# Kernel tuning notes

Hardware: AMD Instinct MI355X
Metric: run time of the kernel (lower is better)

The kernel has to match this reference:

```python
import jax, jax.numpy as jnp
import numpy as np

NEG_SLOPE = 0.2  # LeakyReLU slope used by standard GAT


def setup_inputs() -> dict:
    key = jax.random.key(0)
    k1, k2, k3, k4, k5, k6 = jax.random.split(key, 6)
    N, E, F_in, F_out = 100000, 1600000, 256, 128
    x = jax.random.normal(k1, (N, F_in), dtype=jnp.float32)
    edge_index = jax.random.randint(k2, (2, E), 0, N, dtype=jnp.int32)
    W = jax.random.normal(k3, (F_in, F_out), dtype=jnp.float32) * (1.0 / np.sqrt(F_in))
    a_src = jax.random.normal(k4, (F_out,), dtype=jnp.float32) * 0.1
    a_dst = jax.random.normal(k5, (F_out,), dtype=jnp.float32) * 0.1
    return {"x": x, "edge_index": edge_index, "W": W, "a_src": a_src, "a_dst": a_dst}


def reference(x, edge_index, W, a_src, a_dst):
    N = x.shape[0]
    src, dst = edge_index[0], edge_index[1]

    Wh = x @ W                               # [N, F_out]
    alpha_src = Wh @ a_src                   # [N]
    alpha_dst = Wh @ a_dst                   # [N]

    e = alpha_src[src] + alpha_dst[dst]      # [E] raw edge scores
    e = jnp.where(e > 0, e, NEG_SLOPE * e)   # LeakyReLU(0.2)

    # segment softmax over incoming edges of each destination node
    seg_max = jax.ops.segment_max(e, dst, num_segments=N)          # [N]
    seg_max = jnp.where(jnp.isfinite(seg_max), seg_max, 0.0)
    e_exp = jnp.exp(e - seg_max[dst])                               # [E]
    denom = jax.ops.segment_sum(e_exp, dst, num_segments=N)         # [N]
    alpha = e_exp / (denom[dst] + 1e-16)                            # [E]

    # weighted aggregation of source messages
    msgs = alpha[:, None] * Wh[src]                                  # [E, F_out]
    out = jax.ops.segment_sum(msgs, dst, num_segments=N)             # [N, F_out]
    return jax.nn.elu(out)
```

## Files before the change

### kernel.cpp

```cpp
#include <hip/hip_runtime.h>
#include <math.h>

#define NEG_SLOPE 0.2f
#define BINSH 8
#define BCAP 6144

typedef __attribute__((ext_vector_type(8))) short bf16x8;
typedef __attribute__((ext_vector_type(4))) float f32x4;
typedef __attribute__((ext_vector_type(8))) unsigned short us8;

__device__ inline unsigned short f2b(float f) {
  union { float f; unsigned u; } v; v.f = f;
  unsigned r = v.u + 0x7fffu + ((v.u >> 16) & 1u);
  return (unsigned short)(r >> 16);
}

__device__ inline void gload_lds16(const float* g, void* l) {
  __builtin_amdgcn_global_load_lds(
      (const __attribute__((address_space(1))) void*)g,
      (__attribute__((address_space(3))) void*)l, 16, 0, 0);
}

__launch_bounds__(256)
__global__ void k_work1(const float* __restrict__ W, unsigned short* __restrict__ WtBs,
                        const int* __restrict__ src, const int* __restrict__ dst,
                        int* __restrict__ cursor, unsigned* __restrict__ binned,
                        int E, int NBUK) {
  int bid = blockIdx.x;
  int t = threadIdx.x;
  if (bid < 128) {
    int i = bid * 256 + t;
    int k = i >> 7, n = i & 127;
    int c = k >> 3, e = k & 7;
    WtBs[n * 256 + ((c ^ (n & 31)) << 3) + e] = f2b(W[(size_t)k * 128 + n]);
    return;
  }
  __shared__ int lh[512];
  for (int c = t; c < NBUK; c += 256) lh[c] = 0;
  __syncthreads();
  int base = (bid - 128) * 2048;
  int bq[8], rq[8]; unsigned pq[8];
#pragma unroll
  for (int q = 0; q < 8; ++q) {
    int j = base + q * 256 + t;
    if (j < E) {
      int d = dst[j], s = src[j];
      bq[q] = d >> BINSH;
      pq[q] = ((unsigned)s << 8) | (unsigned)(d & 255);
      rq[q] = atomicAdd(&lh[bq[q]], 1);
    } else bq[q] = -1;
  }
  __syncthreads();
  for (int c = t; c < NBUK; c += 256) { int cnt = lh[c]; if (cnt) lh[c] = atomicAdd(&cursor[c], cnt); }
  __syncthreads();
#pragma unroll
  for (int q = 0; q < 8; ++q)
    if (bq[q] >= 0) binned[(size_t)bq[q] * BCAP + lh[bq[q]] + rq[q]] = pq[q];
}

__launch_bounds__(512, 4)
__global__ void k_work2(const float* __restrict__ x, const unsigned short* __restrict__ WtBs,
                        const float* __restrict__ a_src, const float* __restrict__ a_dst,
                        unsigned short* __restrict__ WhB, float* __restrict__ asrc,
                        float* __restrict__ adst, int N, int nGemm,
                        const unsigned* __restrict__ binned, const int* __restrict__ cursor,
                        int* __restrict__ offsets, int* __restrict__ degs,
                        int* __restrict__ csr) {
  __shared__ __align__(16) unsigned char sbuf[65536];
  int t = threadIdx.x;
  if ((int)blockIdx.x < nGemm) {
    unsigned short* Bs = (unsigned short*)sbuf;
    unsigned short* Cs = (unsigned short*)sbuf;
    int lane = t & 63, wid = t >> 6;
    int lr = lane & 15, lh2 = lane >> 4;
    int m0 = blockIdx.x * 256;

#pragma unroll
    for (int i = 0; i < 8; ++i) {
      int chunk = i * 512 + t;
      gload_lds16((const float*)WtBs + (size_t)chunk * 4, (char*)sbuf + (size_t)chunk * 16);
    }

    int row0 = m0 + wid * 32 + lr;
    int row1 = row0 + 16;
    int r0c = row0 < N ? row0 : N - 1;
    int r1c = row1 < N ? row1 : N - 1;
    const float* xp0 = x + (size_t)r0c * 256 + lh2 * 8;
    const float* xp1 = x + (size_t)r1c * 256 + lh2 * 8;

    f32x4 acc[2][8];
#pragma unroll
    for (int rf = 0; rf < 2; ++rf)
#pragma unroll
      for (int f = 0; f < 8; ++f) acc[rf][f] = (f32x4){0.f, 0.f, 0.f, 0.f};

    __syncthreads();

#pragma unroll
    for (int ks = 0; ks < 8; ++ks) {
      float4 u0 = *(const float4*)(xp0 + ks * 32);
      float4 u1 = *(const float4*)(xp0 + ks * 32 + 4);
      float4 v0 = *(const float4*)(xp1 + ks * 32);
      float4 v1 = *(const float4*)(xp1 + ks * 32 + 4);
      bf16x8 a0, a1;
      a0[0] = (short)f2b(u0.x); a0[1] = (short)f2b(u0.y);
      a0[2] = (short)f2b(u0.z); a0[3] = (short)f2b(u0.w);
      a0[4] = (short)f2b(u1.x); a0[5] = (short)f2b(u1.y);
      a0[6] = (short)f2b(u1.z); a0[7] = (short)f2b(u1.w);
      a1[0] = (short)f2b(v0.x); a1[1] = (short)f2b(v0.y);
      a1[2] = (short)f2b(v0.z); a1[3] = (short)f2b(v0.w);
      a1[4] = (short)f2b(v1.x); a1[5] = (short)f2b(v1.y);
      a1[6] = (short)f2b(v1.z); a1[7] = (short)f2b(v1.w);
#pragma unroll
      for (int f = 0; f < 8; ++f) {
        int n = lr + 16 * f;
        bf16x8 b = *(const bf16x8*)(Bs + n * 256 + (((ks * 4 + lh2) ^ (n & 31)) << 3));
        acc[0][f] = __builtin_amdgcn_mfma_f32_16x16x32_bf16(a0, b, acc[0][f], 0, 0, 0);
        acc[1][f] = __builtin_amdgcn_mfma_f32_16x16x32_bf16(a1, b, acc[1][f], 0, 0, 0);
      }
    }

    float asv[8], adv[8];
#pragma unroll
    for (int f = 0; f < 8; ++f) { asv[f] = a_src[lr + 16 * f]; adv[f] = a_dst[lr + 16 * f]; }
    float as_p[2][4] = {}, ad_p[2][4] = {};
#pragma unroll
    for (int rf = 0; rf < 2; ++rf)
#pragma unroll
      for (int f = 0; f < 8; ++f)
#pragma unroll
        for (int r = 0; r < 4; ++r) {
          as_p[rf][r] += acc[rf][f][r] * asv[f];
          ad_p[rf][r] += acc[rf][f][r] * adv[f];
        }
#pragma unroll
    for (int off = 1; off < 16; off <<= 1)
#pragma unroll
      for (int rf = 0; rf < 2; ++rf)
#pragma unroll
        for (int r = 0; r < 4; ++r) {
          as_p[rf][r] += __shfl_xor(as_p[rf][r], off);
          ad_p[rf][r] += __shfl_xor(ad_p[rf][r], off);
        }
    if (lr == 0) {
#pragma unroll
      for (int rf = 0; rf < 2; ++rf)
#pragma unroll
        for (int r = 0; r < 4; ++r) {
          int m = m0 + wid * 32 + rf * 16 + lh2 * 4 + r;
          if (m < N) { asrc[m] = as_p[rf][r]; adst[m] = ad_p[rf][r]; }
        }
    }

#pragma unroll
    for (int h = 0; h < 2; ++h) {
      __syncthreads();
      if ((wid >> 2) == h) {
#pragma unroll
        for (int rf = 0; rf < 2; ++rf)
#pragma unroll
          for (int f = 0; f < 8; ++f)
#pragma unroll
            for (int r = 0; r < 4; ++r)
              Cs[((wid & 3) * 32 + rf * 16 + lh2 * 4 + r) * 136 + lr + 16 * f] =
                  f2b(acc[rf][f][r]);
      }
      __syncthreads();
#pragma unroll
      for (int i = 0; i < 4; ++i) {
        int chunk = i * 512 + t;
        int row = chunk >> 4, c8 = chunk & 15;
        int m = m0 + h * 128 + row;
        if (m < N)
          *(us8*)(WhB + (size_t)m * 128 + c8 * 8) = *(const us8*)(Cs + row * 136 + c8 * 8);
      }
    }
    return;
  }

  {
    int b = blockIdx.x - nGemm;
    int beg = b * BCAP, end = beg + cursor[b];
    int node0 = b << BINSH;
    int nn = N - node0; if (nn > 256) nn = 256; if (nn < 0) nn = 0;
    int* ldeg = (int*)sbuf;
    int* lcur = ldeg + 256;
    int* wp = lcur + 256;
    if (t < 256) ldeg[t] = 0;
    __syncthreads();
    for (int j = beg + t; j < end; j += 512) atomicAdd(&ldeg[binned[j] & 255u], 1);
    __syncthreads();
    if (t < 256) {
      int lane = t & 63, wid = t >> 6;
      int v = (t < nn) ? ldeg[t] : 0;
      int incl = v;
#pragma unroll
      for (int off = 1; off < 64; off <<= 1) { int u = __shfl_up(incl, off); if (lane >= off) incl += u; }
      if (lane == 63) wp[wid] = incl;
      lcur[t] = incl - v;
    }
    __syncthreads();
    if (t < 256) {
      int wid = t >> 6;
      int add = 0;
      for (int k = 0; k < wid; ++k) add += wp[k];
      int ex = add + lcur[t];
      int v = (t < nn) ? ldeg[t] : 0;
      if (t < nn) { offsets[node0 + t] = beg + ex; degs[node0 + t] = v; }
      lcur[t] = ex;
    }
    __syncthreads();
    for (int j = beg + t; j < end; j += 512) {
      unsigned e = binned[j];
      int r = atomicAdd(&lcur[e & 255u], 1);
      csr[beg + r] = (int)(e >> 8);
    }
  }
}

__launch_bounds__(256)
__global__ void k_agg(const int* __restrict__ csr, const int* __restrict__ offsets,
                      const int* __restrict__ degs,
                      const unsigned short* __restrict__ WhB, const float* __restrict__ asrc,
                      const float* __restrict__ adst, float* __restrict__ out, int N) {
  int gt = blockIdx.x * blockDim.x + threadIdx.x;
  int wave = gt >> 6;
  int lane = gt & 63;
  int lq = lane & 15;
  int g = lane >> 4;
  int node = wave * 4 + g;
  if (node >= N) return;
  int beg = offsets[node];
  int end = beg + degs[node];
  float ad = adst[node];
  float acc[8] = {};
  float psum = 0.f;
  for (int chunk = beg; chunk < end; chunk += 16) {
    int j = chunk + lq;
    float p = 0.f; int mys = 0;
    if (j < end) {
      mys = csr[j];
      float e = asrc[mys] + ad;
      e = e > 0.f ? e : NEG_SLOPE * e;
      p = __expf(e);
    }
    psum += p;
#pragma unroll
    for (int tt = 0; tt < 8; ++tt) {
      float pt = __shfl(p, tt, 16);
      int st = __shfl(mys, tt, 16);
      uint4 v = *(const uint4*)(WhB + (size_t)(unsigned)st * 128u + lq * 8);
      acc[0] = fmaf(pt, __uint_as_float(v.x << 16), acc[0]);
      acc[1] = fmaf(pt, __uint_as_float(v.x & 0xffff0000u), acc[1]);
      acc[2] = fmaf(pt, __uint_as_float(v.y << 16), acc[2]);
      acc[3] = fmaf(pt, __uint_as_float(v.y & 0xffff0000u), acc[3]);
      acc[4] = fmaf(pt, __uint_as_float(v.z << 16), acc[4]);
      acc[5] = fmaf(pt, __uint_as_float(v.z & 0xffff0000u), acc[5]);
      acc[6] = fmaf(pt, __uint_as_float(v.w << 16), acc[6]);
      acc[7] = fmaf(pt, __uint_as_float(v.w & 0xffff0000u), acc[7]);
    }
    __builtin_amdgcn_sched_barrier(0);
#pragma unroll
    for (int tt = 8; tt < 16; ++tt) {
      float pt = __shfl(p, tt, 16);
      int st = __shfl(mys, tt, 16);
      uint4 v = *(const uint4*)(WhB + (size_t)(unsigned)st * 128u + lq * 8);
      acc[0] = fmaf(pt, __uint_as_float(v.x << 16), acc[0]);
      acc[1] = fmaf(pt, __uint_as_float(v.x & 0xffff0000u), acc[1]);
      acc[2] = fmaf(pt, __uint_as_float(v.y << 16), acc[2]);
      acc[3] = fmaf(pt, __uint_as_float(v.y & 0xffff0000u), acc[3]);
      acc[4] = fmaf(pt, __uint_as_float(v.z << 16), acc[4]);
      acc[5] = fmaf(pt, __uint_as_float(v.z & 0xffff0000u), acc[5]);
      acc[6] = fmaf(pt, __uint_as_float(v.w << 16), acc[6]);
      acc[7] = fmaf(pt, __uint_as_float(v.w & 0xffff0000u), acc[7]);
    }
  }
  psum += __shfl_xor(psum, 1);
  psum += __shfl_xor(psum, 2);
  psum += __shfl_xor(psum, 4);
  psum += __shfl_xor(psum, 8);
  float inv = 1.f / (psum + 1e-16f);
  size_t obase = (size_t)node * 128 + lq * 8;
  float r[8];
#pragma unroll
  for (int i = 0; i < 8; ++i) {
    float o = acc[i] * inv;
    r[i] = o > 0.f ? o : __expf(o) - 1.f;
  }
  f32x4 lo = {r[0], r[1], r[2], r[3]};
  f32x4 hi = {r[4], r[5], r[6], r[7]};
  __builtin_nontemporal_store(lo, (f32x4*)(out + obase));
  __builtin_nontemporal_store(hi, (f32x4*)(out + obase + 4));
}

extern "C" void kernel_launch(void* const* d_in, const int* in_sizes, int n_in,
                              void* d_out, int out_size, void* d_ws, size_t ws_size,
                              hipStream_t stream) {
  const float* x = (const float*)d_in[0];
  const int* ei = (const int*)d_in[1];
  const float* W = (const float*)d_in[2];
  const float* a_src = (const float*)d_in[3];
  const float* a_dst = (const float*)d_in[4];
  int N = in_sizes[0] / 256;
  int E = in_sizes[1] / 2;
  const int* src = ei;
  const int* dst = ei + E;
  float* out = (float*)d_out;
  int NBUK = (N + 255) >> BINSH;
  size_t REG = (size_t)NBUK * BCAP;

  unsigned short* WhB = (unsigned short*)d_ws;
  unsigned* binned = (unsigned*)(WhB + (size_t)N * 128);
  int* csr = (int*)(binned + REG);
  float* asrc = (float*)(csr + REG);
  float* adst = asrc + N;
  unsigned short* WtBs = (unsigned short*)(adst + N);
  int* cursor = (int*)(WtBs + 32768);
  int* offsets = cursor + NBUK;
  int* degs = offsets + N;

  int nBinA = (E + 2047) / 2048;
  int nGemm = (N + 255) / 256;

  hipMemsetAsync(cursor, 0, (size_t)NBUK * sizeof(int), stream);
  k_work1<<<128 + nBinA, 256, 0, stream>>>(W, WtBs, src, dst, cursor, binned, E, NBUK);
  k_work2<<<nGemm + NBUK, 512, 0, stream>>>(x, WtBs, a_src, a_dst, WhB, asrc, adst, N, nGemm,
                                            binned, cursor, offsets, degs, csr);
  k_agg<<<(N + 15) / 16, 256, 0, stream>>>(csr, offsets, degs, WhB, asrc, adst, out, N);
}
```

Baseline: 135.8 us.

## Stage x tiles through LDS with async loads and use 1024-thread GEMM blocks

The GEMM part of k_work2 stops reading x straight from global memory into registers. It now streams x in four 64-column stages into a swizzled LDS buffer using global_load_lds, and each of 16 waves computes 16 rows instead of 8 waves computing 32 rows each. Block size doubles to 1024 and LDS grows to 128 KB, so the per-wave accumulator count halves. The cost is two extra barriers per stage with no double buffering, lower occupancy per CU from the larger LDS footprint, and binning blocks that now run 1024 threads on small work.

```diff
diff --git a/kernel.cpp b/kernel.cpp
--- a/kernel.cpp
+++ b/kernel.cpp
@@ -15,7 +15,7 @@
   return (unsigned short)(r >> 16);
 }
 
-__device__ inline void gload_lds16(const float* g, void* l) {
+__device__ inline void gload_lds16(const void* g, void* l) {
   __builtin_amdgcn_global_load_lds(
       (const __attribute__((address_space(1))) void*)g,
       (__attribute__((address_space(3))) void*)l, 16, 0, 0);
@@ -58,7 +58,7 @@
     if (bq[q] >= 0) binned[(size_t)bq[q] * BCAP + lh[bq[q]] + rq[q]] = pq[q];
 }
 
-__launch_bounds__(512, 4)
+__launch_bounds__(1024, 4)
 __global__ void k_work2(const float* __restrict__ x, const unsigned short* __restrict__ WtBs,
                         const float* __restrict__ a_src, const float* __restrict__ a_dst,
                         unsigned short* __restrict__ WhB, float* __restrict__ asrc,
@@ -66,109 +66,100 @@
                         const unsigned* __restrict__ binned, const int* __restrict__ cursor,
                         int* __restrict__ offsets, int* __restrict__ degs,
                         int* __restrict__ csr) {
-  __shared__ __align__(16) unsigned char sbuf[65536];
+  __shared__ __align__(16) unsigned char sbuf[131072];
   int t = threadIdx.x;
   if ((int)blockIdx.x < nGemm) {
     unsigned short* Bs = (unsigned short*)sbuf;
-    unsigned short* Cs = (unsigned short*)sbuf;
+    float* As = (float*)(sbuf + 65536);
+    unsigned short* Cs = (unsigned short*)(sbuf + 65536);
     int lane = t & 63, wid = t >> 6;
     int lr = lane & 15, lh2 = lane >> 4;
     int m0 = blockIdx.x * 256;
 
 #pragma unroll
-    for (int i = 0; i < 8; ++i) {
-      int chunk = i * 512 + t;
-      gload_lds16((const float*)WtBs + (size_t)chunk * 4, (char*)sbuf + (size_t)chunk * 16);
-    }
-
-    int row0 = m0 + wid * 32 + lr;
-    int row1 = row0 + 16;
-    int r0c = row0 < N ? row0 : N - 1;
-    int r1c = row1 < N ? row1 : N - 1;
-    const float* xp0 = x + (size_t)r0c * 256 + lh2 * 8;
-    const float* xp1 = x + (size_t)r1c * 256 + lh2 * 8;
-
-    f32x4 acc[2][8];
-#pragma unroll
-    for (int rf = 0; rf < 2; ++rf)
-#pragma unroll
-      for (int f = 0; f < 8; ++f) acc[rf][f] = (f32x4){0.f, 0.f, 0.f, 0.f};
-
-    __syncthreads();
-
-#pragma unroll
-    for (int ks = 0; ks < 8; ++ks) {
-      float4 u0 = *(const float4*)(xp0 + ks * 32);
-      float4 u1 = *(const float4*)(xp0 + ks * 32 + 4);
-      float4 v0 = *(const float4*)(xp1 + ks * 32);
-      float4 v1 = *(const float4*)(xp1 + ks * 32 + 4);
-      bf16x8 a0, a1;
-      a0[0] = (short)f2b(u0.x); a0[1] = (short)f2b(u0.y);
-      a0[2] = (short)f2b(u0.z); a0[3] = (short)f2b(u0.w);
-      a0[4] = (short)f2b(u1.x); a0[5] = (short)f2b(u1.y);
-      a0[6] = (short)f2b(u1.z); a0[7] = (short)f2b(u1.w);
-      a1[0] = (short)f2b(v0.x); a1[1] = (short)f2b(v0.y);
-      a1[2] = (short)f2b(v0.z); a1[3] = (short)f2b(v0.w);
-      a1[4] = (short)f2b(v1.x); a1[5] = (short)f2b(v1.y);
-      a1[6] = (short)f2b(v1.z); a1[7] = (short)f2b(v1.w);
-#pragma unroll
-      for (int f = 0; f < 8; ++f) {
-        int n = lr + 16 * f;
-        bf16x8 b = *(const bf16x8*)(Bs + n * 256 + (((ks * 4 + lh2) ^ (n & 31)) << 3));
-        acc[0][f] = __builtin_amdgcn_mfma_f32_16x16x32_bf16(a0, b, acc[0][f], 0, 0, 0);
-        acc[1][f] = __builtin_amdgcn_mfma_f32_16x16x32_bf16(a1, b, acc[1][f], 0, 0, 0);
-      }
+    for (int i = 0; i < 4; ++i) {
+      int chunk = i * 1024 + t;
+      gload_lds16((const char*)WtBs + (size_t)chunk * 16, (char*)sbuf + (size_t)chunk * 16);
+    }
+
+    f32x4 acc[8];
+#pragma unroll
+    for (int f = 0; f < 8; ++f) acc[f] = (f32x4){0.f, 0.f, 0.f, 0.f};
+
+    int arow = wid * 16 + lr;
+
+    for (int s = 0; s < 4; ++s) {
+#pragma unroll
+      for (int i = 0; i < 4; ++i) {
+        int chunk = i * 1024 + t;
+        int row = chunk >> 4, c = chunk & 15;
+        int m = m0 + row; if (m >= N) m = N - 1;
+        int cs = c ^ (row & 15);
+        gload_lds16(x + (size_t)m * 256 + s * 64 + cs * 4, (char*)As + (size_t)chunk * 16);
+      }
+      __syncthreads();
+
+#pragma unroll
+      for (int ks2 = 0; ks2 < 2; ++ks2) {
+        int j0 = ks2 * 8 + lh2 * 2;
+        f32x4 u0 = *(const f32x4*)(As + arow * 64 + ((j0 ^ lr) << 2));
+        f32x4 u1 = *(const f32x4*)(As + arow * 64 + (((j0 + 1) ^ lr) << 2));
+        bf16x8 a;
+        a[0] = (short)f2b(u0[0]); a[1] = (short)f2b(u0[1]);
+        a[2] = (short)f2b(u0[2]); a[3] = (short)f2b(u0[3]);
+        a[4] = (short)f2b(u1[0]); a[5] = (short)f2b(u1[1]);
+        a[6] = (short)f2b(u1[2]); a[7] = (short)f2b(u1[3]);
+#pragma unroll
+        for (int f = 0; f < 8; ++f) {
+          int n = lr + 16 * f;
+          bf16x8 b = *(const bf16x8*)(Bs + n * 256 +
+                                      (((s * 8 + ks2 * 4 + lh2) ^ (n & 31)) << 3));
+          acc[f] = __builtin_amdgcn_mfma_f32_16x16x32_bf16(a, b, acc[f], 0, 0, 0);
+        }
+      }
+      __syncthreads();
     }
 
     float asv[8], adv[8];
 #pragma unroll
     for (int f = 0; f < 8; ++f) { asv[f] = a_src[lr + 16 * f]; adv[f] = a_dst[lr + 16 * f]; }
-    float as_p[2][4] = {}, ad_p[2][4] = {};
-#pragma unroll
-    for (int rf = 0; rf < 2; ++rf)
-#pragma unroll
-      for (int f = 0; f < 8; ++f)
-#pragma unroll
-        for (int r = 0; r < 4; ++r) {
-          as_p[rf][r] += acc[rf][f][r] * asv[f];
-          ad_p[rf][r] += acc[rf][f][r] * adv[f];
-        }
+    float as_p[4] = {}, ad_p[4] = {};
+#pragma unroll
+    for (int f = 0; f < 8; ++f)
+#pragma unroll
+      for (int r = 0; r < 4; ++r) {
+        as_p[r] += acc[f][r] * asv[f];
+        ad_p[r] += acc[f][r] * adv[f];
+      }
 #pragma unroll
     for (int off = 1; off < 16; off <<= 1)
 #pragma unroll
-      for (int rf = 0; rf < 2; ++rf)
-#pragma unroll
-        for (int r = 0; r < 4; ++r) {
-          as_p[rf][r] += __shfl_xor(as_p[rf][r], off);
-          ad_p[rf][r] += __shfl_xor(ad_p[rf][r], off);
-        }
+      for (int r = 0; r < 4; ++r) {
+        as_p[r] += __shfl_xor(as_p[r], off);
+        ad_p[r] += __shfl_xor(ad_p[r], off);
+      }
     if (lr == 0) {
 #pragma unroll
-      for (int rf = 0; rf < 2; ++rf)
-#pragma unroll
-        for (int r = 0; r < 4; ++r) {
-          int m = m0 + wid * 32 + rf * 16 + lh2 * 4 + r;
-          if (m < N) { asrc[m] = as_p[rf][r]; adst[m] = ad_p[rf][r]; }
-        }
+      for (int r = 0; r < 4; ++r) {
+        int m = m0 + wid * 16 + lh2 * 4 + r;
+        if (m < N) { asrc[m] = as_p[r]; adst[m] = ad_p[r]; }
+      }
     }
 
 #pragma unroll
     for (int h = 0; h < 2; ++h) {
       __syncthreads();
-      if ((wid >> 2) == h) {
-#pragma unroll
-        for (int rf = 0; rf < 2; ++rf)
-#pragma unroll
-          for (int f = 0; f < 8; ++f)
-#pragma unroll
-            for (int r = 0; r < 4; ++r)
-              Cs[((wid & 3) * 32 + rf * 16 + lh2 * 4 + r) * 136 + lr + 16 * f] =
-                  f2b(acc[rf][f][r]);
+      if ((wid >> 3) == h) {
+#pragma unroll
+        for (int f = 0; f < 8; ++f)
+#pragma unroll
+          for (int r = 0; r < 4; ++r)
+            Cs[((wid & 7) * 16 + lh2 * 4 + r) * 136 + lr + 16 * f] = f2b(acc[f][r]);
       }
       __syncthreads();
 #pragma unroll
-      for (int i = 0; i < 4; ++i) {
-        int chunk = i * 512 + t;
+      for (int i = 0; i < 2; ++i) {
+        int chunk = i * 1024 + t;
         int row = chunk >> 4, c8 = chunk & 15;
         int m = m0 + h * 128 + row;
         if (m < N)
@@ -188,7 +179,7 @@
     int* wp = lcur + 256;
     if (t < 256) ldeg[t] = 0;
     __syncthreads();
-    for (int j = beg + t; j < end; j += 512) atomicAdd(&ldeg[binned[j] & 255u], 1);
+    for (int j = beg + t; j < end; j += 1024) atomicAdd(&ldeg[binned[j] & 255u], 1);
     __syncthreads();
     if (t < 256) {
       int lane = t & 63, wid = t >> 6;
@@ -210,7 +201,7 @@
       lcur[t] = ex;
     }
     __syncthreads();
-    for (int j = beg + t; j < end; j += 512) {
+    for (int j = beg + t; j < end; j += 1024) {
       unsigned e = binned[j];
       int r = atomicAdd(&lcur[e & 255u], 1);
       csr[beg + r] = (int)(e >> 8);
@@ -324,7 +315,7 @@
 
   hipMemsetAsync(cursor, 0, (size_t)NBUK * sizeof(int), stream);
   k_work1<<<128 + nBinA, 256, 0, stream>>>(W, WtBs, src, dst, cursor, binned, E, NBUK);
-  k_work2<<<nGemm + NBUK, 512, 0, stream>>>(x, WtBs, a_src, a_dst, WhB, asrc, adst, N, nGemm,
-                                            binned, cursor, offsets, degs, csr);
+  k_work2<<<nGemm + NBUK, 1024, 0, stream>>>(x, WtBs, a_src, a_dst, WhB, asrc, adst, N, nGemm,
+                                             binned, cursor, offsets, degs, csr);
   k_agg<<<(N + 15) / 16, 256, 0, stream>>>(csr, offsets, degs, WhB, asrc, adst, out, N);
 }
```

After: 141.5 us. 4.2% more time.
